# Kernel optimization log

Measured on AMD Instinct MI355X. Metric: run time of the kernel, lower is better.

Reference implementation:

```python
import jax, jax.numpy as jnp
import numpy as np

N, E = 50000, 800000
IN_DIM, EDGE_DIM, HID, OUT_DIM, L = 128, 16, 64, 8, 4
MSG_EPS = 1e-7  # GENConv eps added to relu(msg)


def layer_norm(x, g, b, eps=1e-5):
    mu = x.mean(-1, keepdims=True)
    var = ((x - mu) ** 2).mean(-1, keepdims=True)
    return (x - mu) * jax.lax.rsqrt(var + eps) * g + b


def segment_softmax(logits, seg, num_segments):
    # numerically stable softmax over edges grouped by destination node
    m = jax.ops.segment_max(logits, seg, num_segments=num_segments)
    m = jnp.where(jnp.isfinite(m), m, 0.0)
    e = jnp.exp(logits - m[seg])
    s = jax.ops.segment_sum(e, seg, num_segments=num_segments)
    return e / (s[seg] + 1e-16)


def gen_conv(x, src, dst, ea, t, W1, b1, g1, be1, W2, b2):
    # GENConv: message = relu(x_j + e_ij) + eps, softmax-aggregate by dst, add root, MLP [h->2h->h]
    msg = jax.nn.relu(x[src] + ea) + MSG_EPS          # [E, H]
    alpha = segment_softmax(msg * t, dst, x.shape[0]) # [E, H]
    agg = jax.ops.segment_sum(msg * alpha, dst, num_segments=x.shape[0])  # [N, H]
    h = agg + x
    h = jax.nn.relu(layer_norm(h @ W1 + b1, g1, be1))  # [N, 2H]
    return h @ W2 + b2                                 # [N, H]


def setup_inputs() -> dict:
    key = jax.random.key(0)
    ks = jax.random.split(key, 16)
    sc = 0.05
    inp = {
        "x": jax.random.normal(ks[0], (N, IN_DIM), jnp.float32),
        "edge_attr": jax.random.normal(ks[1], (E, EDGE_DIM), jnp.float32),
        "node_W": jax.random.normal(ks[2], (IN_DIM, HID), jnp.float32) * sc,
        "node_b": jnp.zeros((HID,), jnp.float32),
        "edge_W": jax.random.normal(ks[3], (EDGE_DIM, HID), jnp.float32) * sc,
        "edge_b": jnp.zeros((HID,), jnp.float32),
        "conv_t": jnp.ones((L,), jnp.float32),
        "conv_W1": jax.random.normal(ks[4], (L, HID, 2 * HID), jnp.float32) * sc,
        "conv_b1": jnp.zeros((L, 2 * HID), jnp.float32),
        "conv_g1": jnp.ones((L, 2 * HID), jnp.float32),
        "conv_be1": jnp.zeros((L, 2 * HID), jnp.float32),
        "conv_W2": jax.random.normal(ks[5], (L, 2 * HID, HID), jnp.float32) * sc,
        "conv_b2": jnp.zeros((L, HID), jnp.float32),
        "ln_g": jnp.ones((L, HID), jnp.float32),
        "ln_b": jnp.zeros((L, HID), jnp.float32),
        "lin_W": jax.random.normal(ks[6], (HID, OUT_DIM), jnp.float32) * sc,
        "lin_b": jnp.zeros((OUT_DIM,), jnp.float32),
        "edge_index": jax.random.randint(ks[7], (2, E), 0, N, jnp.int64),
    }
    return inp


def reference(x, edge_attr, node_W, node_b, edge_W, edge_b,
              conv_t, conv_W1, conv_b1, conv_g1, conv_be1, conv_W2, conv_b2,
              ln_g, ln_b, lin_W, lin_b, edge_index):
    src, dst = edge_index[0], edge_index[1]  # flow: source_to_target
    h = x @ node_W + node_b
    ea = edge_attr @ edge_W + edge_b
    # first layer: conv only (DeeperGCN applies layers[0].conv directly)
    h = gen_conv(h, src, dst, ea, conv_t[0], conv_W1[0], conv_b1[0],
                 conv_g1[0], conv_be1[0], conv_W2[0], conv_b2[0])
    # res+ blocks: x + conv(dropout(relu(norm(x)))); dropout inactive (eval)
    for i in range(1, L):
        z = jax.nn.relu(layer_norm(h, ln_g[i], ln_b[i]))
        h = h + gen_conv(z, src, dst, ea, conv_t[i], conv_W1[i], conv_b1[i],
                         conv_g1[i], conv_be1[i], conv_W2[i], conv_b2[i])
    h = jax.nn.relu(layer_norm(h, ln_g[0], ln_b[0]))
    return h @ lin_W + lin_b
```

## Files before the change

kernel.cpp:

```cpp
#include <hip/hip_runtime.h>
#include <hip/hip_fp16.h>

#define N_NODES 50000
#define N_EDGES 800000
#define IN_DIM  128
#define EDGE_DIM 16
#define HID     64
#define HID2    128
#define OUT_DIM 8
#define N_LAYERS 4
#define SCAN_BLOCKS 196

typedef _Float16 half8 __attribute__((ext_vector_type(8)));
typedef float floatx4 __attribute__((ext_vector_type(4)));

__global__ __launch_bounds__(256, 4) void hist_kernel(
    const int* __restrict__ dsts, int* __restrict__ deg)
{
    const int e = blockIdx.x * 256 + threadIdx.x;
    atomicAdd(&deg[dsts[e]], 1);
}

__global__ __launch_bounds__(256) void scan1_kernel(
    const int* __restrict__ deg, int* __restrict__ bsum)
{
    __shared__ int red[256];
    const int i = blockIdx.x * 256 + threadIdx.x;
    red[threadIdx.x] = (i < N_NODES) ? deg[i] : 0;
    __syncthreads();
    for (int off = 128; off > 0; off >>= 1) {
        if (threadIdx.x < off) red[threadIdx.x] += red[threadIdx.x + off];
        __syncthreads();
    }
    if (threadIdx.x == 0) bsum[blockIdx.x] = red[0];
}

__global__ __launch_bounds__(256, 1) void scan2_kernel(
    const int* __restrict__ bsum, int* __restrict__ bbase)
{
    __shared__ int part[256];
    const int t = threadIdx.x;
    int v = (t < SCAN_BLOCKS) ? bsum[t] : 0;
    part[t] = v;
    __syncthreads();
    for (int off = 1; off < 256; off <<= 1) {
        int x = (t >= off) ? part[t - off] : 0;
        __syncthreads();
        part[t] += x;
        __syncthreads();
    }
    bbase[t] = (t > 0) ? part[t - 1] : 0;
}

__global__ __launch_bounds__(256) void scan3_kernel(
    const int* __restrict__ deg, const int* __restrict__ bbase,
    int* __restrict__ cursor)
{
    __shared__ int part[256];
    const int t = threadIdx.x;
    const int i = blockIdx.x * 256 + t;
    const int v = (i < N_NODES) ? deg[i] : 0;
    part[t] = v;
    __syncthreads();
    for (int off = 1; off < 256; off <<= 1) {
        int x = (t >= off) ? part[t - off] : 0;
        __syncthreads();
        part[t] += x;
        __syncthreads();
    }
    if (i < N_NODES) cursor[i] = part[t] - v + bbase[blockIdx.x];
}

__global__ __launch_bounds__(256, 4) void scatter_kernel(
    const int* __restrict__ srcs, const int* __restrict__ dsts,
    int* __restrict__ cursor, int* __restrict__ inv, int2* __restrict__ sd)
{
    const int e = blockIdx.x * 256 + threadIdx.x;
    const int d = dsts[e];
    const int pos = atomicAdd(&cursor[d], 1);
    inv[e] = pos;
    sd[pos] = make_int2(srcs[e], d);
}

__global__ __launch_bounds__(256, 2) void node_proj_kernel(
    const float* __restrict__ x, const float* __restrict__ W,
    const float* __restrict__ b, float* __restrict__ h, __half* __restrict__ zh)
{
    __shared__ float xs[4][IN_DIM];
    const int c = threadIdx.x & 63;
    const int local_n = threadIdx.x >> 6;
    float w[IN_DIM];
#pragma unroll
    for (int k = 0; k < IN_DIM; ++k) w[k] = W[k * HID + c];
    const float bias = b[c];

    for (int base = blockIdx.x * 4; base < N_NODES; base += gridDim.x * 4) {
        __syncthreads();
#pragma unroll
        for (int i = 0; i < 2; ++i) {
            int idx = threadIdx.x + i * 256;
            int nn = idx >> 7, kk = idx & 127;
            xs[nn][kk] = x[(base + nn) * IN_DIM + kk];
        }
        __syncthreads();
        const int n = base + local_n;
        float acc = bias;
#pragma unroll
        for (int k4 = 0; k4 < IN_DIM / 4; ++k4) {
            float4 xv = ((const float4*)xs[local_n])[k4];
            acc = fmaf(xv.x, w[k4 * 4 + 0], acc);
            acc = fmaf(xv.y, w[k4 * 4 + 1], acc);
            acc = fmaf(xv.z, w[k4 * 4 + 2], acc);
            acc = fmaf(xv.w, w[k4 * 4 + 3], acc);
        }
        h[n * HID + c] = acc;
        zh[n * HID + c] = __float2half(acc);
    }
}

__global__ __launch_bounds__(256, 4) void edge_emb_kernel(
    const float* __restrict__ ea, const float* __restrict__ W,
    const float* __restrict__ b, const int* __restrict__ inv,
    __half* __restrict__ eah)
{
    __shared__ __half lds_t[4][16 * HID];
    const int lane = threadIdx.x & 63;
    const int waveid = threadIdx.x >> 6;
    const int wave = (blockIdx.x * 256 + threadIdx.x) >> 6;
    const int nwaves = gridDim.x * 4;
    const int m = lane & 15, q = lane >> 4;
    const int NT = N_EDGES / 16;

    half8 bf[4];
#pragma unroll
    for (int blk = 0; blk < 4; ++blk) {
#pragma unroll
        for (int i = 0; i < 8; ++i) {
            const int k = q * 8 + i;
            bf[blk][i] = (k < EDGE_DIM)
                ? (_Float16)W[k * HID + blk * 16 + m] : (_Float16)0.f;
        }
    }
    float bv[4];
#pragma unroll
    for (int blk = 0; blk < 4; ++blk) bv[blk] = b[blk * 16 + m];

    const int ed = lane >> 3, ch = lane & 7;

    for (int tile = wave; tile < NT; tile += nwaves) {
        const int e0 = tile * 16;
        half8 af;
#pragma unroll
        for (int i = 0; i < 8; ++i) af[i] = (_Float16)0.f;
        if (q < 2) {
            const float4* ap =
                (const float4*)(ea + (size_t)(e0 + m) * EDGE_DIM + q * 8);
            const float4 lo = ap[0];
            const float4 hi = ap[1];
            af[0] = (_Float16)lo.x; af[1] = (_Float16)lo.y;
            af[2] = (_Float16)lo.z; af[3] = (_Float16)lo.w;
            af[4] = (_Float16)hi.x; af[5] = (_Float16)hi.y;
            af[6] = (_Float16)hi.z; af[7] = (_Float16)hi.w;
        }
        floatx4 c[4];
#pragma unroll
        for (int blk = 0; blk < 4; ++blk) {
            floatx4 cin = {bv[blk], bv[blk], bv[blk], bv[blk]};
            c[blk] = __builtin_amdgcn_mfma_f32_16x16x32_f16(
                af, bf[blk], cin, 0, 0, 0);
        }
#pragma unroll
        for (int blk = 0; blk < 4; ++blk)
#pragma unroll
            for (int r = 0; r < 4; ++r)
                lds_t[waveid][(q * 4 + r) * HID + blk * 16 + m] =
                    __float2half(c[blk][r]);
        const int pos0 = inv[e0 + ed];
        const int pos1 = inv[e0 + 8 + ed];
        const float4 v0 =
            *(const float4*)&lds_t[waveid][ed * HID + ch * 8];
        const float4 v1 =
            *(const float4*)&lds_t[waveid][(8 + ed) * HID + ch * 8];
        ((float4*)(eah + (size_t)pos0 * HID))[ch] = v0;
        ((float4*)(eah + (size_t)pos1 * HID))[ch] = v1;
    }
}

__global__ __launch_bounds__(256, 4) void edge_agg_kernel(
    const __half* __restrict__ zh, const __half* __restrict__ eah,
    const int2* __restrict__ sd,
    const float* __restrict__ conv_t, int layer,
    float* __restrict__ p, float* __restrict__ s)
{
    const int lane = threadIdx.x & 63;
    const int wave = (blockIdx.x * 256 + threadIdx.x) >> 6;
    const int nwaves = gridDim.x * 4;
    const float t2 = conv_t[layer] * 1.4426950408889634f;
    const int NT = N_EDGES / 64;

    const _Float16* zf = (const _Float16*)zh;
    const _Float16* ef = (const _Float16*)eah;

    for (int tile = wave; tile < NT; tile += nwaves) {
        const int e0 = tile * 64;
        const int2 sdv = sd[e0 + lane];
        const int sv = sdv.x;
        const int dv = sdv.y;
        const int pv = __shfl_up(dv, 1, 64);
        const unsigned long long bmask = __ballot(dv != pv) & ~1ull;
        const _Float16* erow = ef + (size_t)e0 * HID + lane;

        _Float16 za[8], ez[8], zb[8], eb[8];
#pragma unroll
        for (int k = 0; k < 8; ++k) {
            const int a = __builtin_amdgcn_readlane(sv, k);
            za[k] = (zf + (size_t)a * HID)[lane];
            ez[k] = erow[(size_t)k * HID];
        }

        float S = 0.f, P = 0.f;
        int cur = __builtin_amdgcn_readlane(dv, 0);
#pragma unroll
        for (int g = 0; g < 8; ++g) {
            if (g < 7) {
#pragma unroll
                for (int k = 0; k < 8; ++k) {
                    const int a = __builtin_amdgcn_readlane(sv, (g + 1) * 8 + k);
                    zb[k] = (zf + (size_t)a * HID)[lane];
                    eb[k] = erow[(size_t)((g + 1) * 8 + k) * HID];
                }
            }
#pragma unroll
            for (int k = 0; k < 8; ++k) {
                const int j = g * 8 + k;
                if (bmask & (1ull << j)) {
                    unsafeAtomicAdd(&s[(size_t)cur * HID + lane], S);
                    unsafeAtomicAdd(&p[(size_t)cur * HID + lane], P);
                    S = 0.f; P = 0.f;
                    cur = __builtin_amdgcn_readlane(dv, j);
                }
                _Float16 mh = za[k] + ez[k];
                mh = mh > (_Float16)0.f ? mh : (_Float16)0.f;
                const float m = (float)mh + 1e-7f;
                const float xx = __builtin_amdgcn_exp2f(m * t2);
                S += xx;
                P = fmaf(m, xx, P);
            }
            if (g < 7) {
#pragma unroll
                for (int k = 0; k < 8; ++k) { za[k] = zb[k]; ez[k] = eb[k]; }
            }
        }
        unsafeAtomicAdd(&s[(size_t)cur * HID + lane], S);
        unsafeAtomicAdd(&p[(size_t)cur * HID + lane], P);
    }
}

__global__ __launch_bounds__(256, 2) void node_mm1_kernel(
    float* __restrict__ p, float* __restrict__ s,
    const __half* __restrict__ zh,
    const float* __restrict__ W1, const float* __restrict__ b1,
    const float* __restrict__ g1, const float* __restrict__ be1,
    __half* __restrict__ vh)
{
    __shared__ float hs[2][HID];
    __shared__ float red[2][2][2];
    const int j = threadIdx.x & 127;
    const int local_n = threadIdx.x >> 7;
    const int wavehalf = (threadIdx.x >> 6) & 1;
    float w[HID];
#pragma unroll
    for (int k = 0; k < HID; ++k) w[k] = W1[k * HID2 + j];
    const float bias = b1[j];
    const float g = g1[j];
    const float be = be1[j];

    for (int base = blockIdx.x * 2; base < N_NODES; base += gridDim.x * 2) {
        __syncthreads();
        if (threadIdx.x < 128) {
            int nn = threadIdx.x >> 6, c = threadIdx.x & 63;
            int idx = (base + nn) * HID + c;
            hs[nn][c] = p[idx] / (s[idx] + 1e-16f) + __half2float(zh[idx]);
            p[idx] = 0.f;
            s[idx] = 0.f;
        }
        __syncthreads();
        const int n = base + local_n;
        float u = bias;
#pragma unroll
        for (int k4 = 0; k4 < HID / 4; ++k4) {
            float4 hv = ((const float4*)hs[local_n])[k4];
            u = fmaf(hv.x, w[k4 * 4 + 0], u);
            u = fmaf(hv.y, w[k4 * 4 + 1], u);
            u = fmaf(hv.z, w[k4 * 4 + 2], u);
            u = fmaf(hv.w, w[k4 * 4 + 3], u);
        }
        float ps_ = u;
#pragma unroll
        for (int o = 1; o < 64; o <<= 1) ps_ += __shfl_xor(ps_, o, 64);
        if ((threadIdx.x & 63) == 0) red[local_n][0][wavehalf] = ps_;
        __syncthreads();
        const float mu = (red[local_n][0][0] + red[local_n][0][1]) * (1.f / 128.f);
        const float d = u - mu;
        float q = d * d;
#pragma unroll
        for (int o = 1; o < 64; o <<= 1) q += __shfl_xor(q, o, 64);
        if ((threadIdx.x & 63) == 0) red[local_n][1][wavehalf] = q;
        __syncthreads();
        const float var = (red[local_n][1][0] + red[local_n][1][1]) * (1.f / 128.f);
        const float y = d * rsqrtf(var + 1e-5f) * g + be;
        vh[(size_t)n * HID2 + j] = __float2half(y > 0.f ? y : 0.f);
    }
}

__global__ __launch_bounds__(256, 2) void node_mm2_kernel(
    const __half* __restrict__ vh,
    const float* __restrict__ W2, const float* __restrict__ b2,
    const float* __restrict__ lng, const float* __restrict__ lnb,
    float* __restrict__ h, __half* __restrict__ zh, int residual)
{
    __shared__ float vs[4][HID2];
    const int c = threadIdx.x & 63;
    const int local_n = threadIdx.x >> 6;
    float w[HID2];
#pragma unroll
    for (int k = 0; k < HID2; ++k) w[k] = W2[k * HID + c];
    const float bias = b2[c];
    const float g = lng[c];
    const float be = lnb[c];

    for (int base = blockIdx.x * 4; base < N_NODES; base += gridDim.x * 4) {
        __syncthreads();
        {
            const __half2* vp = (const __half2*)(vh + (size_t)base * HID2);
            const float2 f = __half22float2(vp[threadIdx.x]);
            const int nn = threadIdx.x >> 6, kk = (threadIdx.x & 63) * 2;
            vs[nn][kk] = f.x;
            vs[nn][kk + 1] = f.y;
        }
        __syncthreads();
        const int n = base + local_n;
        float acc = bias;
#pragma unroll
        for (int k4 = 0; k4 < HID2 / 4; ++k4) {
            float4 vv = ((const float4*)vs[local_n])[k4];
            acc = fmaf(vv.x, w[k4 * 4 + 0], acc);
            acc = fmaf(vv.y, w[k4 * 4 + 1], acc);
            acc = fmaf(vv.z, w[k4 * 4 + 2], acc);
            acc = fmaf(vv.w, w[k4 * 4 + 3], acc);
        }
        const float hn = residual ? (h[n * HID + c] + acc) : acc;
        h[n * HID + c] = hn;
        float ps_ = hn;
#pragma unroll
        for (int o = 1; o < 64; o <<= 1) ps_ += __shfl_xor(ps_, o, 64);
        const float mu = ps_ * (1.f / 64.f);
        const float d = hn - mu;
        float q = d * d;
#pragma unroll
        for (int o = 1; o < 64; o <<= 1) q += __shfl_xor(q, o, 64);
        const float var = q * (1.f / 64.f);
        const float y = d * rsqrtf(var + 1e-5f) * g + be;
        zh[n * HID + c] = __float2half(y > 0.f ? y : 0.f);
    }
}

__global__ __launch_bounds__(256, 4) void final_kernel(
    const __half* __restrict__ zh, const float* __restrict__ Wl,
    const float* __restrict__ bl, float* __restrict__ out)
{
    __shared__ float wl[HID * OUT_DIM];
    for (int i = threadIdx.x; i < HID * OUT_DIM; i += 256) wl[i] = Wl[i];
    __syncthreads();
    const int total = N_NODES * OUT_DIM;
    for (int idx = blockIdx.x * 256 + threadIdx.x; idx < total;
         idx += gridDim.x * 256) {
        const int n = idx >> 3, o = idx & 7;
        const __half2* zp = (const __half2*)(zh + (size_t)n * HID);
        float acc = bl[o];
#pragma unroll
        for (int k2 = 0; k2 < HID / 2; ++k2) {
            const float2 f = __half22float2(zp[k2]);
            acc = fmaf(f.x, wl[(k2 * 2 + 0) * OUT_DIM + o], acc);
            acc = fmaf(f.y, wl[(k2 * 2 + 1) * OUT_DIM + o], acc);
        }
        out[idx] = acc;
    }
}

extern "C" void kernel_launch(void* const* d_in, const int* in_sizes, int n_in,
                              void* d_out, int out_size, void* d_ws, size_t ws_size,
                              hipStream_t stream)
{
    const float* x         = (const float*)d_in[0];
    const float* edge_attr = (const float*)d_in[1];
    const float* node_W    = (const float*)d_in[2];
    const float* node_b    = (const float*)d_in[3];
    const float* edge_W    = (const float*)d_in[4];
    const float* edge_b    = (const float*)d_in[5];
    const float* conv_t    = (const float*)d_in[6];
    const float* conv_W1   = (const float*)d_in[7];
    const float* conv_b1   = (const float*)d_in[8];
    const float* conv_g1   = (const float*)d_in[9];
    const float* conv_be1  = (const float*)d_in[10];
    const float* conv_W2   = (const float*)d_in[11];
    const float* conv_b2   = (const float*)d_in[12];
    const float* ln_g      = (const float*)d_in[13];
    const float* ln_b      = (const float*)d_in[14];
    const float* lin_W     = (const float*)d_in[15];
    const float* lin_b     = (const float*)d_in[16];
    const int*   edge_index= (const int*)d_in[17];
    const int*   srcs = edge_index;
    const int*   dsts = edge_index + N_EDGES;
    float* out = (float*)d_out;

    float* h   = (float*)d_ws;
    float* p   = h   + N_NODES * HID;
    float* s   = p   + N_NODES * HID;
    __half* vh  = (__half*)(s + N_NODES * HID);
    __half* zh  = vh + (size_t)N_NODES * HID2;
    __half* eah = zh + (size_t)N_NODES * HID;
    int* deg     = (int*)(eah + (size_t)N_EDGES * HID);
    int* cursor  = deg + N_NODES;
    int* bsum    = cursor + N_NODES;
    int* bbase   = bsum + 256;
    int* inv     = bbase + 256;
    int2* sd     = (int2*)(inv + N_EDGES);

    hipMemsetAsync(deg, 0, (size_t)N_NODES * sizeof(int), stream);
    hist_kernel<<<N_EDGES / 256, 256, 0, stream>>>(dsts, deg);
    scan1_kernel<<<SCAN_BLOCKS, 256, 0, stream>>>(deg, bsum);
    scan2_kernel<<<1, 256, 0, stream>>>(bsum, bbase);
    scan3_kernel<<<SCAN_BLOCKS, 256, 0, stream>>>(deg, bbase, cursor);
    scatter_kernel<<<N_EDGES / 256, 256, 0, stream>>>(srcs, dsts, cursor, inv, sd);

    node_proj_kernel<<<2048, 256, 0, stream>>>(x, node_W, node_b, h, zh);
    edge_emb_kernel<<<3125, 256, 0, stream>>>(edge_attr, edge_W, edge_b, inv, eah);

    hipMemsetAsync(p, 0, (size_t)2 * N_NODES * HID * sizeof(float), stream);

    for (int layer = 0; layer < N_LAYERS; ++layer) {
        edge_agg_kernel<<<3125, 256, 0, stream>>>(zh, eah, sd,
                                                  conv_t, layer, p, s);
        node_mm1_kernel<<<2048, 256, 0, stream>>>(
            p, s, zh,
            conv_W1 + (size_t)layer * HID * HID2, conv_b1 + layer * HID2,
            conv_g1 + layer * HID2, conv_be1 + layer * HID2, vh);
        const float* gz = (layer < N_LAYERS - 1) ? (ln_g + (layer + 1) * HID) : ln_g;
        const float* bz = (layer < N_LAYERS - 1) ? (ln_b + (layer + 1) * HID) : ln_b;
        node_mm2_kernel<<<2048, 256, 0, stream>>>(
            vh, conv_W2 + (size_t)layer * HID2 * HID, conv_b2 + layer * HID,
            gz, bz, h, zh, layer > 0 ? 1 : 0);
    }
    final_kernel<<<1024, 256, 0, stream>>>(zh, lin_W, lin_b, out);
}
```

Before: 795.3 us.

## Replace atomic CSR build with two-level bucket sort and packed indices

Builds the destination-sorted edge order with a coarse bucket histogram and scatter followed by a per-bucket shared-memory counting sort, replacing per-node global atomics and a three-kernel scan. Source and destination are packed into one 32-bit word, and the edge embedding gathers inputs by edge id so it can write output rows contiguously. It reduces global atomic contention and kernel count in preprocessing. The per-bucket LDS buffer assumes at most 4096 edges per 128-node bucket, and the 16-bit packing assumes node ids below 65536.

```diff
diff --git a/kernel.cpp b/kernel.cpp
--- a/kernel.cpp
+++ b/kernel.cpp
@@ -9,77 +9,122 @@
 #define HID2    128
 #define OUT_DIM 8
 #define N_LAYERS 4
-#define SCAN_BLOCKS 196
+#define NBUCK   391
+#define CCHUNK  4096
+#define CBLOCKS 196
 
 typedef _Float16 half8 __attribute__((ext_vector_type(8)));
 typedef float floatx4 __attribute__((ext_vector_type(4)));
 
-__global__ __launch_bounds__(256, 4) void hist_kernel(
-    const int* __restrict__ dsts, int* __restrict__ deg)
-{
-    const int e = blockIdx.x * 256 + threadIdx.x;
-    atomicAdd(&deg[dsts[e]], 1);
-}
-
-__global__ __launch_bounds__(256) void scan1_kernel(
-    const int* __restrict__ deg, int* __restrict__ bsum)
-{
-    __shared__ int red[256];
-    const int i = blockIdx.x * 256 + threadIdx.x;
-    red[threadIdx.x] = (i < N_NODES) ? deg[i] : 0;
-    __syncthreads();
-    for (int off = 128; off > 0; off >>= 1) {
-        if (threadIdx.x < off) red[threadIdx.x] += red[threadIdx.x + off];
-        __syncthreads();
-    }
-    if (threadIdx.x == 0) bsum[blockIdx.x] = red[0];
-}
-
-__global__ __launch_bounds__(256, 1) void scan2_kernel(
-    const int* __restrict__ bsum, int* __restrict__ bbase)
-{
-    __shared__ int part[256];
+__global__ __launch_bounds__(256, 4) void chist_kernel(
+    const int* __restrict__ dsts, int* __restrict__ ccnt)
+{
+    __shared__ int lh[NBUCK];
+    for (int i = threadIdx.x; i < NBUCK; i += 256) lh[i] = 0;
+    __syncthreads();
+    const int base = blockIdx.x * CCHUNK;
+#pragma unroll
+    for (int i = 0; i < 16; ++i) {
+        const int e = base + i * 256 + threadIdx.x;
+        if (e < N_EDGES) atomicAdd(&lh[dsts[e] >> 7], 1);
+    }
+    __syncthreads();
+    for (int i = threadIdx.x; i < NBUCK; i += 256)
+        if (lh[i]) atomicAdd(&ccnt[i], lh[i]);
+}
+
+__global__ __launch_bounds__(256, 1) void cscan_kernel(
+    const int* __restrict__ ccnt, int* __restrict__ coff, int* __restrict__ ccur)
+{
+    __shared__ int part[512];
     const int t = threadIdx.x;
-    int v = (t < SCAN_BLOCKS) ? bsum[t] : 0;
-    part[t] = v;
-    __syncthreads();
-    for (int off = 1; off < 256; off <<= 1) {
-        int x = (t >= off) ? part[t - off] : 0;
-        __syncthreads();
-        part[t] += x;
-        __syncthreads();
-    }
-    bbase[t] = (t > 0) ? part[t - 1] : 0;
-}
-
-__global__ __launch_bounds__(256) void scan3_kernel(
-    const int* __restrict__ deg, const int* __restrict__ bbase,
-    int* __restrict__ cursor)
-{
-    __shared__ int part[256];
-    const int t = threadIdx.x;
-    const int i = blockIdx.x * 256 + t;
-    const int v = (i < N_NODES) ? deg[i] : 0;
-    part[t] = v;
-    __syncthreads();
-    for (int off = 1; off < 256; off <<= 1) {
-        int x = (t >= off) ? part[t - off] : 0;
-        __syncthreads();
-        part[t] += x;
-        __syncthreads();
-    }
-    if (i < N_NODES) cursor[i] = part[t] - v + bbase[blockIdx.x];
-}
-
-__global__ __launch_bounds__(256, 4) void scatter_kernel(
+    part[t]       = (t < NBUCK)       ? ccnt[t]       : 0;
+    part[t + 256] = (t + 256 < NBUCK) ? ccnt[t + 256] : 0;
+    __syncthreads();
+    for (int off = 1; off < 512; off <<= 1) {
+        const int v0 = (t >= off) ? part[t - off] : 0;
+        const int v1 = (t + 256 >= off) ? part[t + 256 - off] : 0;
+        __syncthreads();
+        part[t] += v0; part[t + 256] += v1;
+        __syncthreads();
+    }
+    if (t < NBUCK) { const int ex = (t > 0) ? part[t - 1] : 0; coff[t] = ex; ccur[t] = ex; }
+    const int i2 = t + 256;
+    if (i2 < NBUCK) { coff[i2] = part[i2 - 1]; ccur[i2] = part[i2 - 1]; }
+    if (t == 0) coff[NBUCK] = part[NBUCK - 1];
+}
+
+__global__ __launch_bounds__(256, 4) void cscatter_kernel(
     const int* __restrict__ srcs, const int* __restrict__ dsts,
-    int* __restrict__ cursor, int* __restrict__ inv, int2* __restrict__ sd)
-{
-    const int e = blockIdx.x * 256 + threadIdx.x;
-    const int d = dsts[e];
-    const int pos = atomicAdd(&cursor[d], 1);
-    inv[e] = pos;
-    sd[pos] = make_int2(srcs[e], d);
+    int* __restrict__ ccur, uint2* __restrict__ tmp)
+{
+    __shared__ int lh[NBUCK], lbase[NBUCK], lrank[NBUCK];
+    for (int i = threadIdx.x; i < NBUCK; i += 256) { lh[i] = 0; lrank[i] = 0; }
+    __syncthreads();
+    const int base = blockIdx.x * CCHUNK;
+    int myd[16], mys[16];
+#pragma unroll
+    for (int i = 0; i < 16; ++i) {
+        const int e = base + i * 256 + threadIdx.x;
+        if (e < N_EDGES) {
+            myd[i] = dsts[e]; mys[i] = srcs[e];
+            atomicAdd(&lh[myd[i] >> 7], 1);
+        } else myd[i] = -1;
+    }
+    __syncthreads();
+    for (int i = threadIdx.x; i < NBUCK; i += 256) {
+        const int c = lh[i];
+        lbase[i] = c ? atomicAdd(&ccur[i], c) : 0;
+    }
+    __syncthreads();
+#pragma unroll
+    for (int i = 0; i < 16; ++i) {
+        if (myd[i] >= 0) {
+            const int e = base + i * 256 + threadIdx.x;
+            const int b = myd[i] >> 7;
+            const int r = atomicAdd(&lrank[b], 1);
+            tmp[lbase[b] + r] =
+                make_uint2((unsigned)mys[i] | ((unsigned)myd[i] << 16),
+                           (unsigned)e);
+        }
+    }
+}
+
+__global__ __launch_bounds__(256, 1) void fsort_kernel(
+    const uint2* __restrict__ tmp, const int* __restrict__ coff,
+    unsigned* __restrict__ sd2, int* __restrict__ eid)
+{
+    __shared__ uint2 ebuf[4096];
+    __shared__ int lh[128], lsc[128];
+    const int b = blockIdx.x;
+    const int lo = coff[b];
+    const int cnt = coff[b + 1] - lo;
+    if (threadIdx.x < 128) lh[threadIdx.x] = 0;
+    __syncthreads();
+    for (int i = threadIdx.x; i < cnt; i += 256) {
+        const uint2 v = tmp[lo + i];
+        ebuf[i] = v;
+        atomicAdd(&lh[(int)(v.x >> 16) - b * 128], 1);
+    }
+    __syncthreads();
+    if (threadIdx.x < 128) lsc[threadIdx.x] = lh[threadIdx.x];
+    __syncthreads();
+    for (int off = 1; off < 128; off <<= 1) {
+        int v = 0;
+        if (threadIdx.x < 128 && threadIdx.x >= off) v = lsc[threadIdx.x - off];
+        __syncthreads();
+        if (threadIdx.x < 128) lsc[threadIdx.x] += v;
+        __syncthreads();
+    }
+    if (threadIdx.x < 128) lh[threadIdx.x] = lsc[threadIdx.x] - lh[threadIdx.x];
+    __syncthreads();
+    for (int i = threadIdx.x; i < cnt; i += 256) {
+        const uint2 v = ebuf[i];
+        const int d = (int)(v.x >> 16) - b * 128;
+        const int pos = atomicAdd(&lh[d], 1);
+        sd2[lo + pos] = v.x;
+        eid[lo + pos] = (int)v.y;
+    }
 }
 
 __global__ __launch_bounds__(256, 2) void node_proj_kernel(
@@ -120,7 +165,7 @@
 
 __global__ __launch_bounds__(256, 4) void edge_emb_kernel(
     const float* __restrict__ ea, const float* __restrict__ W,
-    const float* __restrict__ b, const int* __restrict__ inv,
+    const float* __restrict__ b, const int* __restrict__ eid,
     __half* __restrict__ eah)
 {
     __shared__ __half lds_t[4][16 * HID];
@@ -149,12 +194,13 @@
 
     for (int tile = wave; tile < NT; tile += nwaves) {
         const int e0 = tile * 16;
+        const int eidx = eid[e0 + m];
         half8 af;
 #pragma unroll
         for (int i = 0; i < 8; ++i) af[i] = (_Float16)0.f;
         if (q < 2) {
             const float4* ap =
-                (const float4*)(ea + (size_t)(e0 + m) * EDGE_DIM + q * 8);
+                (const float4*)(ea + (size_t)eidx * EDGE_DIM + q * 8);
             const float4 lo = ap[0];
             const float4 hi = ap[1];
             af[0] = (_Float16)lo.x; af[1] = (_Float16)lo.y;
@@ -175,20 +221,18 @@
             for (int r = 0; r < 4; ++r)
                 lds_t[waveid][(q * 4 + r) * HID + blk * 16 + m] =
                     __float2half(c[blk][r]);
-        const int pos0 = inv[e0 + ed];
-        const int pos1 = inv[e0 + 8 + ed];
         const float4 v0 =
             *(const float4*)&lds_t[waveid][ed * HID + ch * 8];
         const float4 v1 =
             *(const float4*)&lds_t[waveid][(8 + ed) * HID + ch * 8];
-        ((float4*)(eah + (size_t)pos0 * HID))[ch] = v0;
-        ((float4*)(eah + (size_t)pos1 * HID))[ch] = v1;
+        ((float4*)(eah + (size_t)(e0 + ed) * HID))[ch] = v0;
+        ((float4*)(eah + (size_t)(e0 + 8 + ed) * HID))[ch] = v1;
     }
 }
 
 __global__ __launch_bounds__(256, 4) void edge_agg_kernel(
     const __half* __restrict__ zh, const __half* __restrict__ eah,
-    const int2* __restrict__ sd,
+    const unsigned* __restrict__ sd2,
     const float* __restrict__ conv_t, int layer,
     float* __restrict__ p, float* __restrict__ s)
 {
@@ -203,9 +247,9 @@
 
     for (int tile = wave; tile < NT; tile += nwaves) {
         const int e0 = tile * 64;
-        const int2 sdv = sd[e0 + lane];
-        const int sv = sdv.x;
-        const int dv = sdv.y;
+        const unsigned sdv = sd2[e0 + lane];
+        const int sv = (int)(sdv & 0xffffu);
+        const int dv = (int)(sdv >> 16);
         const int pv = __shfl_up(dv, 1, 64);
         const unsigned long long bmask = __ballot(dv != pv) & ~1ull;
         const _Float16* erow = ef + (size_t)e0 * HID + lane;
@@ -420,27 +464,26 @@
     __half* vh  = (__half*)(s + N_NODES * HID);
     __half* zh  = vh + (size_t)N_NODES * HID2;
     __half* eah = zh + (size_t)N_NODES * HID;
-    int* deg     = (int*)(eah + (size_t)N_EDGES * HID);
-    int* cursor  = deg + N_NODES;
-    int* bsum    = cursor + N_NODES;
-    int* bbase   = bsum + 256;
-    int* inv     = bbase + 256;
-    int2* sd     = (int2*)(inv + N_EDGES);
-
-    hipMemsetAsync(deg, 0, (size_t)N_NODES * sizeof(int), stream);
-    hist_kernel<<<N_EDGES / 256, 256, 0, stream>>>(dsts, deg);
-    scan1_kernel<<<SCAN_BLOCKS, 256, 0, stream>>>(deg, bsum);
-    scan2_kernel<<<1, 256, 0, stream>>>(bsum, bbase);
-    scan3_kernel<<<SCAN_BLOCKS, 256, 0, stream>>>(deg, bbase, cursor);
-    scatter_kernel<<<N_EDGES / 256, 256, 0, stream>>>(srcs, dsts, cursor, inv, sd);
+    uint2* tmp  = (uint2*)(eah + (size_t)N_EDGES * HID);
+    unsigned* sd2 = (unsigned*)(tmp + N_EDGES);
+    int* eid    = (int*)(sd2 + N_EDGES);
+    int* ccnt   = eid + N_EDGES;
+    int* coff   = ccnt + NBUCK;
+    int* ccur   = coff + NBUCK + 1;
+
+    hipMemsetAsync(ccnt, 0, (size_t)NBUCK * sizeof(int), stream);
+    chist_kernel<<<CBLOCKS, 256, 0, stream>>>(dsts, ccnt);
+    cscan_kernel<<<1, 256, 0, stream>>>(ccnt, coff, ccur);
+    cscatter_kernel<<<CBLOCKS, 256, 0, stream>>>(srcs, dsts, ccur, tmp);
+    fsort_kernel<<<NBUCK, 256, 0, stream>>>(tmp, coff, sd2, eid);
 
     node_proj_kernel<<<2048, 256, 0, stream>>>(x, node_W, node_b, h, zh);
-    edge_emb_kernel<<<3125, 256, 0, stream>>>(edge_attr, edge_W, edge_b, inv, eah);
+    edge_emb_kernel<<<3125, 256, 0, stream>>>(edge_attr, edge_W, edge_b, eid, eah);
 
     hipMemsetAsync(p, 0, (size_t)2 * N_NODES * HID * sizeof(float), stream);
 
     for (int layer = 0; layer < N_LAYERS; ++layer) {
-        edge_agg_kernel<<<3125, 256, 0, stream>>>(zh, eah, sd,
+        edge_agg_kernel<<<3125, 256, 0, stream>>>(zh, eah, sd2,
                                                   conv_t, layer, p, s);
         node_mm1_kernel<<<2048, 256, 0, stream>>>(
             p, s, zh,
```

After: 755.0 us. 1.05x faster.
